# Performance work log

Measured on AMD Instinct MI355X. Metric: run time of the kernel, lower is better.

The kernel has to match this reference:

```python
import jax, jax.numpy as jnp
import numpy as np

N_NODES = 20000
N_EDGES = 320000
F_IN = 256      # num_features_mol
HIDDEN = 512    # hidden_size


def _glorot(key, shape):
    fan_in, fan_out = shape
    lim = jnp.sqrt(6.0 / (fan_in + fan_out)).astype(jnp.float32)
    return jax.random.uniform(key, shape, jnp.float32, -lim, lim)


def setup_inputs() -> dict:
    key = jax.random.key(0)
    ks = jax.random.split(key, 12)
    x = jax.random.normal(ks[0], (N_NODES, F_IN), jnp.float32)
    edge_index = jax.random.randint(ks[1], (2, N_EDGES), 0, N_NODES, dtype=jnp.int64)
    d1, d2, d3 = F_IN * 2, F_IN * 2, F_IN * 4  # 512, 512, 1024
    return {
        "x": x,
        "edge_index": edge_index,
        # SAGEConv layer i: lin_l (neighbor, with bias), lin_r (root, no bias)
        "Wl1": _glorot(ks[2], (F_IN, d1)), "bl1": jnp.zeros((d1,), jnp.float32),
        "Wr1": _glorot(ks[3], (F_IN, d1)),
        "Wl2": _glorot(ks[4], (d1, d2)), "bl2": jnp.zeros((d2,), jnp.float32),
        "Wr2": _glorot(ks[5], (d1, d2)),
        "Wl3": _glorot(ks[6], (d2, d3)), "bl3": jnp.zeros((d3,), jnp.float32),
        "Wr3": _glorot(ks[7], (d2, d3)),
        # mol_fc_g1: Linear(4*F -> hidden)
        "Wfc": _glorot(ks[8], (d3, HIDDEN)), "bfc": jnp.zeros((HIDDEN,), jnp.float32),
    }


def _sage_mean(x, src, dst, Wl, bl, Wr):
    # mean-aggregate neighbor features: messages flow src -> dst
    msg = x[src]                                               # [E, d]
    agg = jax.ops.segment_sum(msg, dst, num_segments=N_NODES)  # [N, d]
    cnt = jax.ops.segment_sum(jnp.ones((src.shape[0],), x.dtype), dst,
                              num_segments=N_NODES)            # [N]
    mean = agg / jnp.maximum(cnt, 1.0)[:, None]                # zero-deg -> 0
    return mean @ Wl + bl + x @ Wr


def reference(x, edge_index, Wl1, bl1, Wr1, Wl2, bl2, Wr2, Wl3, bl3, Wr3, Wfc, bfc):
    src, dst = edge_index[0], edge_index[1]
    h = jax.nn.relu(_sage_mean(x, src, dst, Wl1, bl1, Wr1))
    h = jax.nn.relu(_sage_mean(h, src, dst, Wl2, bl2, Wr2))
    h = jax.nn.relu(_sage_mean(h, src, dst, Wl3, bl3, Wr3))
    return h @ Wfc + bfc                                       # [N, HIDDEN]
```

## Files before the change

kernel.cpp:

```cpp
#include <hip/hip_runtime.h>
#include <hip/hip_bf16.h>


typedef __bf16 bf16x8 __attribute__((ext_vector_type(8)));
typedef float  f32x4  __attribute__((ext_vector_type(4)));

#define N_NODES 20000
#define N_EDGES 320000
#define MPAD 20096

__device__ __forceinline__ int clampi(int v, int lo, int hi) {
    return v < lo ? lo : (v > hi ? hi : v);
}

__device__ __forceinline__ void load16_lds(const void* g, void* l) {
    __builtin_amdgcn_global_load_lds(
        (const __attribute__((address_space(1))) void*)g,
        (__attribute__((address_space(3))) void*)l, 16, 0, 0);
}


__global__ void k_count(const int* __restrict__ ei, int E, int* __restrict__ cnt) {
    int e = blockIdx.x * blockDim.x + threadIdx.x;
    if (e < E) atomicAdd(&cnt[clampi(ei[E + e], 0, N_NODES - 1)], 1);
}

__global__ __launch_bounds__(1024) void k_scan_block(const int* __restrict__ cnt,
                                                     int* __restrict__ off,
                                                     int* __restrict__ bsum, int n) {
    __shared__ int sm[1024];
    int b = blockIdx.x, tid = threadIdx.x;
    int i = b * 1024 + tid;
    int v = (i < n) ? cnt[i] : 0;
    sm[tid] = v;
    __syncthreads();
    for (int s = 1; s < 1024; s <<= 1) {
        int t = (tid >= s) ? sm[tid - s] : 0;
        __syncthreads();
        sm[tid] += t;
        __syncthreads();
    }
    if (i < n) off[i] = sm[tid] - v;
    if (tid == 1023) bsum[b] = sm[1023];
}

__global__ void k_scan_carry(const int* __restrict__ bsum, int* __restrict__ carry,
                             int nb, int* __restrict__ off, int n) {
    if (threadIdx.x == 0 && blockIdx.x == 0) {
        int acc = 0;
        for (int b = 0; b < nb; ++b) { carry[b] = acc; acc += bsum[b]; }
        off[n] = acc;
    }
}

__global__ __launch_bounds__(1024) void k_scan_add(int* __restrict__ off,
                                                   int* __restrict__ cur,
                                                   const int* __restrict__ carry, int n) {
    int i = blockIdx.x * 1024 + threadIdx.x;
    if (i < n) {
        int v = off[i] + carry[blockIdx.x];
        off[i] = v;
        cur[i] = v;
    }
}

__global__ void k_fill(const int* __restrict__ ei, int E,
                       int* __restrict__ cur, int* __restrict__ csr) {
    int e = blockIdx.x * blockDim.x + threadIdx.x;
    if (e < E) {
        int dst = clampi(ei[E + e], 0, N_NODES - 1);
        int src = clampi(ei[e], 0, N_NODES - 1);
        int pos = atomicAdd(&cur[dst], 1);
        if (pos >= 0 && pos < E) csr[pos] = src;
    }
}


struct TDesc { const float* W; __bf16* Wt; int K, N, KT, koff, tile0; };
struct TDescs { TDesc d[7]; };

__global__ void k_transpose_all(TDescs ds) {
    __shared__ float tile[32][33];
    int b = blockIdx.x;
    int di = 0;
#pragma unroll
    for (int i = 1; i < 7; ++i)
        if (b >= ds.d[i].tile0) di = i;
    const float* W = ds.d[di].W;
    __bf16* Wt = ds.d[di].Wt;
    int N = ds.d[di].N, KT = ds.d[di].KT, koff = ds.d[di].koff;
    int t = b - ds.d[di].tile0;
    int ntn = N >> 5;
    int nb = (t % ntn) * 32, kb = (t / ntn) * 32;
    for (int i = 0; i < 32; i += 8) {
        int k = kb + threadIdx.y + i, n = nb + threadIdx.x;
        tile[threadIdx.y + i][threadIdx.x] = W[(size_t)k * N + n];
    }
    __syncthreads();
    for (int i = 0; i < 32; i += 8) {
        int n = nb + threadIdx.y + i, k = koff + kb + threadIdx.x;
        size_t o = (size_t)(n >> 7) * ((size_t)KT * 128) + (size_t)(k >> 3) * 1024 +
                   (size_t)((n & 127) * 8) + (k & 7);
        Wt[o] = (__bf16)tile[threadIdx.x][threadIdx.y + i];
    }
}


__global__ __launch_bounds__(256) void k_agg_f32(const float* __restrict__ xin,
                                                 const int* __restrict__ off,
                                                 const int* __restrict__ csr,
                                                 __bf16* __restrict__ acat) {
    __shared__ float sm[4][256];
    int node = blockIdx.x;
    int tid = threadIdx.x, slot = tid >> 6, lane = tid & 63;
    int c0 = lane * 4;
    int beg = off[node], end = off[node + 1];
    float a0 = 0.f, a1 = 0.f, a2 = 0.f, a3 = 0.f;
    for (int e = beg + slot; e < end; e += 4) {
        int s = csr[e];
        float4 v = *(const float4*)(xin + (size_t)s * 256 + c0);
        a0 += v.x; a1 += v.y; a2 += v.z; a3 += v.w;
    }
    sm[slot][c0] = a0; sm[slot][c0 + 1] = a1; sm[slot][c0 + 2] = a2; sm[slot][c0 + 3] = a3;
    __syncthreads();
    __bf16* base = acat + (size_t)(node >> 7) * (512 * 128) + (size_t)((node & 127) * 8);
    if (tid < 32) {
        float inv = 1.f / fmaxf((float)(end - beg), 1.f);
        int c = tid;
        __bf16 tmp[8];
#pragma unroll
        for (int i = 0; i < 8; ++i) {
            int col = c * 8 + i;
            tmp[i] = (__bf16)((sm[0][col] + sm[1][col] + sm[2][col] + sm[3][col]) * inv);
        }
        *(uint4*)(base + (size_t)c * 1024) = *(const uint4*)tmp;
    } else if (tid >= 64 && tid < 96) {
        int c = tid - 64;
        float4 u = *(const float4*)(xin + (size_t)node * 256 + c * 8);
        float4 w = *(const float4*)(xin + (size_t)node * 256 + c * 8 + 4);
        __bf16 tmp[8] = {(__bf16)u.x, (__bf16)u.y, (__bf16)u.z, (__bf16)u.w,
                         (__bf16)w.x, (__bf16)w.y, (__bf16)w.z, (__bf16)w.w};
        *(uint4*)(base + (size_t)(32 + c) * 1024) = *(const uint4*)tmp;
    }
}

__global__ __launch_bounds__(256) void k_agg_bf16(const __hip_bfloat16* __restrict__ hrm,
                                                  const int* __restrict__ off,
                                                  const int* __restrict__ csr,
                                                  __bf16* __restrict__ acat) {
    __shared__ float sm[4][512];
    int node = blockIdx.x;
    int tid = threadIdx.x, slot = tid >> 6, lane = tid & 63;
    int c0 = lane * 8;
    int beg = off[node], end = off[node + 1];
    float a[8] = {};
    for (int e = beg + slot; e < end; e += 4) {
        int s = csr[e];
        uint4 v = *(const uint4*)(hrm + (size_t)s * 512 + c0);
        const __hip_bfloat16* hb = (const __hip_bfloat16*)&v;
#pragma unroll
        for (int j = 0; j < 8; ++j) a[j] += __bfloat162float(hb[j]);
    }
#pragma unroll
    for (int j = 0; j < 8; ++j) sm[slot][c0 + j] = a[j];
    __syncthreads();
    if (tid < 64) {
        float inv = 1.f / fmaxf((float)(end - beg), 1.f);
        int c = tid;
        __bf16 tmp[8];
#pragma unroll
        for (int i = 0; i < 8; ++i) {
            int col = c * 8 + i;
            tmp[i] = (__bf16)((sm[0][col] + sm[1][col] + sm[2][col] + sm[3][col]) * inv);
        }
        *(uint4*)(acat + (size_t)(node >> 7) * (1024 * 128) +
                  (size_t)((node & 127) * 8) + (size_t)c * 1024) = *(const uint4*)tmp;
    }
}


template <bool RELU, int OUTMODE>
__global__ __launch_bounds__(256) void k_gemm(const __bf16* __restrict__ A, int K, int M,
                                              const __bf16* __restrict__ B,
                                              const float* __restrict__ bias,
                                              __bf16* __restrict__ osw, int Kc, int coff,
                                              __bf16* __restrict__ orm, int ldrm,
                                              float* __restrict__ of32, int ldf,
                                              int rtiles, int ctlog2) {
    constexpr int SMEM = (OUTMODE == 2) ? 34816 : 32768;
    __shared__ char smem[SMEM];
    __bf16* Alds = (__bf16*)smem;
    __bf16* Blds = (__bf16*)(smem + 16384);

    int bid = blockIdx.x;
    int xcd = bid & 7, local = bid >> 3;
    int cmask = (1 << ctlog2) - 1;
    int colTile = local & cmask;
    int rowTile = (local >> ctlog2) * 8 + xcd;
    if (rowTile >= rtiles) return;

    const __bf16* Atile = A + (size_t)rowTile * ((size_t)K * 128);
    const __bf16* Btile = B + (size_t)colTile * ((size_t)K * 128);

    int tid = threadIdx.x;
    int wave = tid >> 6, lane = tid & 63;
    int wr = wave >> 1, wc = wave & 1;
    int quad = lane >> 4, l16 = lane & 15;

    f32x4 acc[4][4] = {};

    for (int k0 = 0; k0 < K; k0 += 64) {
        __syncthreads();
        const __bf16* gA = Atile + (size_t)k0 * 128;
        const __bf16* gB = Btile + (size_t)k0 * 128;
#pragma unroll
        for (int j = 0; j < 4; ++j) {
            int slot = (j * 256 + tid) * 8;
            load16_lds(gA + slot, Alds + slot);
            load16_lds(gB + slot, Blds + slot);
        }
        __syncthreads();
#pragma unroll
        for (int sp = 0; sp < 2; ++sp) {
            bf16x8 af[4], bf[4];
#pragma unroll
            for (int mi = 0; mi < 4; ++mi)
                af[mi] = *(const bf16x8*)(Alds + sp * 4096 + quad * 1024 +
                                          (wr * 64 + mi * 16 + l16) * 8);
#pragma unroll
            for (int ni = 0; ni < 4; ++ni)
                bf[ni] = *(const bf16x8*)(Blds + sp * 4096 + quad * 1024 +
                                          (wc * 64 + ni * 16 + l16) * 8);
#pragma unroll
            for (int mi = 0; mi < 4; ++mi)
#pragma unroll
                for (int ni = 0; ni < 4; ++ni)
                    acc[mi][ni] = __builtin_amdgcn_mfma_f32_16x16x32_bf16(
                        af[mi], bf[ni], acc[mi][ni], 0, 0, 0);
        }
    }

    int col0 = colTile * 128;
    int row0 = rowTile * 128;
    __syncthreads();

    if (OUTMODE != 2) {
        __bf16* cb = (__bf16*)smem;
#pragma unroll
        for (int ni = 0; ni < 4; ++ni) {
            int ct = wc * 64 + ni * 16 + l16;
            float bv = bias[col0 + ct];
#pragma unroll
            for (int mi = 0; mi < 4; ++mi) {
                int rb = wr * 64 + mi * 16 + quad * 4;
#pragma unroll
                for (int r = 0; r < 4; ++r) {
                    float v = acc[mi][ni][r] + bv;
                    if (RELU) v = fmaxf(v, 0.f);
                    cb[(ct >> 3) * 1024 + (rb + r) * 8 + (ct & 7)] = (__bf16)v;
                }
            }
        }
        __syncthreads();
        __bf16* dst = osw + (size_t)rowTile * ((size_t)Kc * 128) +
                      (size_t)((coff + col0) >> 3) * 1024;
#pragma unroll
        for (int p2 = 0; p2 < 8; ++p2) {
            int idx = (p2 * 256 + tid) * 8;
            *(uint4*)(dst + idx) = *(const uint4*)(cb + idx);
        }
        if (OUTMODE == 1) {
#pragma unroll
            for (int p2 = 0; p2 < 8; ++p2) {
                int rr = p2 * 16 + (tid >> 4);
                int cc = tid & 15;
                *(uint4*)(orm + (size_t)(row0 + rr) * ldrm + col0 + cc * 8) =
                    *(const uint4*)(cb + cc * 1024 + rr * 8);
            }
        }
    } else {
        float* cf = (float*)smem;
#pragma unroll
        for (int h = 0; h < 2; ++h) {
            if (wc == h) {
#pragma unroll
                for (int ni = 0; ni < 4; ++ni) {
                    int ctl = ni * 16 + l16;
                    float bv = bias[col0 + h * 64 + ctl];
#pragma unroll
                    for (int mi = 0; mi < 4; ++mi) {
                        int rb = wr * 64 + mi * 16 + quad * 4;
#pragma unroll
                        for (int r = 0; r < 4; ++r) {
                            float v = acc[mi][ni][r] + bv;
                            if (RELU) v = fmaxf(v, 0.f);
                            cf[(rb + r) * 68 + ctl] = v;
                        }
                    }
                }
            }
            __syncthreads();
            int chunk = tid & 15, rl = tid >> 4;
#pragma unroll
            for (int p2 = 0; p2 < 8; ++p2) {
                int rt = p2 * 16 + rl;
                int row = row0 + rt;
                if (row < M) {
                    float4 v = *(const float4*)(cf + rt * 68 + chunk * 4);
                    *(float4*)(of32 + (size_t)row * ldf + col0 + h * 64 + chunk * 4) = v;
                }
            }
            __syncthreads();
        }
    }
}


extern "C" void kernel_launch(void* const* d_in, const int* in_sizes, int n_in,
                              void* d_out, int out_size, void* d_ws, size_t ws_size,
                              hipStream_t stream) {
    const float* x   = (const float*)d_in[0];
    const int*   ei  = (const int*)d_in[1];
    const float* Wl1 = (const float*)d_in[2];
    const float* bl1 = (const float*)d_in[3];
    const float* Wr1 = (const float*)d_in[4];
    const float* Wl2 = (const float*)d_in[5];
    const float* bl2 = (const float*)d_in[6];
    const float* Wr2 = (const float*)d_in[7];
    const float* Wl3 = (const float*)d_in[8];
    const float* bl3 = (const float*)d_in[9];
    const float* Wr3 = (const float*)d_in[10];
    const float* Wfc = (const float*)d_in[11];
    const float* bfc = (const float*)d_in[12];
    float* out = (float*)d_out;

    const int NN = N_NODES, E = N_EDGES;
    const int NB = (NN + 1023) / 1024;

    char* p = (char*)d_ws;
    auto alloc = [&](size_t bytes) {
        char* r = p;
        p += (bytes + 511) & ~(size_t)511;
        return r;
    };
    int* cnt   = (int*)alloc((size_t)NN * 4);
    int* off   = (int*)alloc((size_t)(NN + 1) * 4);
    int* cur   = (int*)alloc((size_t)NN * 4);
    int* csr   = (int*)alloc((size_t)E * 4);
    int* bsum  = (int*)alloc((size_t)NB * 4);
    int* carry = (int*)alloc((size_t)NB * 4);
    __bf16* Acat1 = (__bf16*)alloc((size_t)MPAD * 512 * 2);
    __bf16* Acat2 = (__bf16*)alloc((size_t)MPAD * 1024 * 2);
    __bf16* Acat3 = (__bf16*)alloc((size_t)MPAD * 1024 * 2);
    __bf16* Hrm   = (__bf16*)alloc((size_t)MPAD * 512 * 2);
    __bf16* Wt1 = (__bf16*)alloc((size_t)512 * 512 * 2);
    __bf16* Wt2 = (__bf16*)alloc((size_t)512 * 1024 * 2);
    __bf16* Wt3 = (__bf16*)alloc((size_t)1024 * 1024 * 2);
    __bf16* Wt4 = (__bf16*)alloc((size_t)512 * 1024 * 2);
    __bf16* H3 = Acat2;

    hipMemsetAsync(cnt, 0, (size_t)NN * 4, stream);
    k_count<<<(E + 255) / 256, 256, 0, stream>>>(ei, E, cnt);
    k_scan_block<<<NB, 1024, 0, stream>>>(cnt, off, bsum, NN);
    k_scan_carry<<<1, 64, 0, stream>>>(bsum, carry, NB, off, NN);
    k_scan_add<<<NB, 1024, 0, stream>>>(off, cur, carry, NN);
    k_fill<<<(E + 255) / 256, 256, 0, stream>>>(ei, E, cur, csr);

    TDescs td;
    td.d[0] = {Wl1, Wt1, 256, 512, 512, 0, 0};
    td.d[1] = {Wr1, Wt1, 256, 512, 512, 256, 128};
    td.d[2] = {Wl2, Wt2, 512, 512, 1024, 0, 256};
    td.d[3] = {Wr2, Wt2, 512, 512, 1024, 512, 512};
    td.d[4] = {Wl3, Wt3, 512, 1024, 1024, 0, 768};
    td.d[5] = {Wr3, Wt3, 512, 1024, 1024, 512, 1280};
    td.d[6] = {Wfc, Wt4, 1024, 512, 1024, 0, 1792};
    k_transpose_all<<<2304, dim3(32, 8), 0, stream>>>(td);

    int rtiles = (NN + 127) / 128;
    int rg = ((rtiles + 7) / 8) * 8;

    k_agg_f32<<<NN, 256, 0, stream>>>(x, off, csr, Acat1);
    k_gemm<true, 1><<<rg * 4, 256, 0, stream>>>(
        Acat1, 512, NN, Wt1, bl1, Acat2, 1024, 512, Hrm, 512, nullptr, 0, rtiles, 2);

    k_agg_bf16<<<NN, 256, 0, stream>>>((const __hip_bfloat16*)Hrm, off, csr, Acat2);
    k_gemm<true, 1><<<rg * 4, 256, 0, stream>>>(
        Acat2, 1024, NN, Wt2, bl2, Acat3, 1024, 512, Hrm, 512, nullptr, 0, rtiles, 2);

    k_agg_bf16<<<NN, 256, 0, stream>>>((const __hip_bfloat16*)Hrm, off, csr, Acat3);
    k_gemm<true, 0><<<rg * 8, 256, 0, stream>>>(
        Acat3, 1024, NN, Wt3, bl3, H3, 1024, 0, nullptr, 0, nullptr, 0, rtiles, 3);

    k_gemm<false, 2><<<rg * 4, 256, 0, stream>>>(
        H3, 1024, NN, Wt4, bfc, nullptr, 0, 0, nullptr, 0, out, 512, rtiles, 2);
}
```

Measured before the change: 449.9 us.

## Pre-convert x to bf16 and use one wave per node in aggregation

Adds a kernel that converts the fp32 input features to a row-major bf16 copy and writes the root half of the first concat buffer. Layer-1 aggregation then gathers bf16 rows instead of fp32, halving gather bytes. All aggregation kernels switch from one block per node with a 4-way LDS reduction to one wave per node that walks its edge list sequentially, two edges per iteration. This removes shared-memory reductions and block syncs but lowers per-node memory parallelism for high-degree nodes and adds an extra conversion pass.

```diff
diff --git a/kernel.cpp b/kernel.cpp
--- a/kernel.cpp
+++ b/kernel.cpp
@@ -106,75 +106,69 @@
 }
 
 
-__global__ __launch_bounds__(256) void k_agg_f32(const float* __restrict__ xin,
-                                                 const int* __restrict__ off,
-                                                 const int* __restrict__ csr,
-                                                 __bf16* __restrict__ acat) {
-    __shared__ float sm[4][256];
-    int node = blockIdx.x;
-    int tid = threadIdx.x, slot = tid >> 6, lane = tid & 63;
-    int c0 = lane * 4;
+__global__ __launch_bounds__(256) void k_x2bf(const float* __restrict__ x,
+                                              __bf16* __restrict__ xrm,
+                                              __bf16* __restrict__ acat) {
+    int tid = threadIdx.x;
+    int node = blockIdx.x * 8 + (tid >> 5);
+    int f0 = (tid & 31) * 8;
+    float4 u = *(const float4*)(x + (size_t)node * 256 + f0);
+    float4 w = *(const float4*)(x + (size_t)node * 256 + f0 + 4);
+    alignas(16) __bf16 tmp[8] = {(__bf16)u.x, (__bf16)u.y, (__bf16)u.z, (__bf16)u.w,
+                                 (__bf16)w.x, (__bf16)w.y, (__bf16)w.z, (__bf16)w.w};
+    *(uint4*)(xrm + (size_t)node * 256 + f0) = *(const uint4*)tmp;
+    *(uint4*)(acat + (size_t)(node >> 7) * (512 * 128) +
+              (size_t)(32 + (f0 >> 3)) * 1024 + (size_t)((node & 127) * 8)) =
+        *(const uint4*)tmp;
+}
+
+
+template <int D, int KC>
+__global__ __launch_bounds__(256) void k_agg(const __hip_bfloat16* __restrict__ hrm,
+                                             const int* __restrict__ off,
+                                             const int* __restrict__ csr,
+                                             __bf16* __restrict__ acat) {
+    constexpr int FPL = D / 64;
+    int wave = threadIdx.x >> 6, lane = threadIdx.x & 63;
+    int node = blockIdx.x * 4 + wave;
+    int c0 = lane * FPL;
     int beg = off[node], end = off[node + 1];
-    float a0 = 0.f, a1 = 0.f, a2 = 0.f, a3 = 0.f;
-    for (int e = beg + slot; e < end; e += 4) {
-        int s = csr[e];
-        float4 v = *(const float4*)(xin + (size_t)s * 256 + c0);
-        a0 += v.x; a1 += v.y; a2 += v.z; a3 += v.w;
-    }
-    sm[slot][c0] = a0; sm[slot][c0 + 1] = a1; sm[slot][c0 + 2] = a2; sm[slot][c0 + 3] = a3;
-    __syncthreads();
-    __bf16* base = acat + (size_t)(node >> 7) * (512 * 128) + (size_t)((node & 127) * 8);
-    if (tid < 32) {
-        float inv = 1.f / fmaxf((float)(end - beg), 1.f);
-        int c = tid;
-        __bf16 tmp[8];
-#pragma unroll
-        for (int i = 0; i < 8; ++i) {
-            int col = c * 8 + i;
-            tmp[i] = (__bf16)((sm[0][col] + sm[1][col] + sm[2][col] + sm[3][col]) * inv);
-        }
-        *(uint4*)(base + (size_t)c * 1024) = *(const uint4*)tmp;
-    } else if (tid >= 64 && tid < 96) {
-        int c = tid - 64;
-        float4 u = *(const float4*)(xin + (size_t)node * 256 + c * 8);
-        float4 w = *(const float4*)(xin + (size_t)node * 256 + c * 8 + 4);
-        __bf16 tmp[8] = {(__bf16)u.x, (__bf16)u.y, (__bf16)u.z, (__bf16)u.w,
-                         (__bf16)w.x, (__bf16)w.y, (__bf16)w.z, (__bf16)w.w};
-        *(uint4*)(base + (size_t)(32 + c) * 1024) = *(const uint4*)tmp;
-    }
-}
-
-__global__ __launch_bounds__(256) void k_agg_bf16(const __hip_bfloat16* __restrict__ hrm,
-                                                  const int* __restrict__ off,
-                                                  const int* __restrict__ csr,
-                                                  __bf16* __restrict__ acat) {
-    __shared__ float sm[4][512];
-    int node = blockIdx.x;
-    int tid = threadIdx.x, slot = tid >> 6, lane = tid & 63;
-    int c0 = lane * 8;
-    int beg = off[node], end = off[node + 1];
-    float a[8] = {};
-    for (int e = beg + slot; e < end; e += 4) {
-        int s = csr[e];
-        uint4 v = *(const uint4*)(hrm + (size_t)s * 512 + c0);
-        const __hip_bfloat16* hb = (const __hip_bfloat16*)&v;
+    float a[FPL] = {};
+
+    auto accum = [&](int s) {
+        if constexpr (FPL == 8) {
+            uint4 v = *(const uint4*)(hrm + (size_t)s * D + c0);
+            const __hip_bfloat16* hb = (const __hip_bfloat16*)&v;
 #pragma unroll
         for (int j = 0; j < 8; ++j) a[j] += __bfloat162float(hb[j]);
-    }
-#pragma unroll
-    for (int j = 0; j < 8; ++j) sm[slot][c0 + j] = a[j];
-    __syncthreads();
-    if (tid < 64) {
-        float inv = 1.f / fmaxf((float)(end - beg), 1.f);
-        int c = tid;
-        __bf16 tmp[8];
-#pragma unroll
-        for (int i = 0; i < 8; ++i) {
-            int col = c * 8 + i;
-            tmp[i] = (__bf16)((sm[0][col] + sm[1][col] + sm[2][col] + sm[3][col]) * inv);
-        }
-        *(uint4*)(acat + (size_t)(node >> 7) * (1024 * 128) +
-                  (size_t)((node & 127) * 8) + (size_t)c * 1024) = *(const uint4*)tmp;
+        } else {
+            uint2 v = *(const uint2*)(hrm + (size_t)s * D + c0);
+            const __hip_bfloat16* hb = (const __hip_bfloat16*)&v;
+#pragma unroll
+            for (int j = 0; j < 4; ++j) a[j] += __bfloat162float(hb[j]);
+        }
+    };
+
+    int e = beg;
+    for (; e + 1 < end; e += 2) {
+        int s0 = csr[e], s1 = csr[e + 1];
+        accum(s0);
+        accum(s1);
+    }
+    if (e < end) accum(csr[e]);
+
+    float inv = 1.f / fmaxf((float)(end - beg), 1.f);
+    alignas(16) __bf16 tmp[FPL];
+#pragma unroll
+    for (int j = 0; j < FPL; ++j) tmp[j] = (__bf16)(a[j] * inv);
+
+    __bf16* base = acat + (size_t)(node >> 7) * ((size_t)KC * 128) +
+                   (size_t)((node & 127) * 8);
+    if constexpr (FPL == 8) {
+        *(uint4*)(base + (size_t)lane * 1024) = *(const uint4*)tmp;
+    } else {
+        *(uint2*)(base + (size_t)(lane >> 1) * 1024 + (size_t)((lane & 1) * 4)) =
+            *(const uint2*)tmp;
     }
 }
 
@@ -353,11 +347,14 @@
     __bf16* Acat2 = (__bf16*)alloc((size_t)MPAD * 1024 * 2);
     __bf16* Acat3 = (__bf16*)alloc((size_t)MPAD * 1024 * 2);
     __bf16* Hrm   = (__bf16*)alloc((size_t)MPAD * 512 * 2);
+    __bf16* Xrm   = (__bf16*)alloc((size_t)MPAD * 256 * 2);
     __bf16* Wt1 = (__bf16*)alloc((size_t)512 * 512 * 2);
     __bf16* Wt2 = (__bf16*)alloc((size_t)512 * 1024 * 2);
     __bf16* Wt3 = (__bf16*)alloc((size_t)1024 * 1024 * 2);
     __bf16* Wt4 = (__bf16*)alloc((size_t)512 * 1024 * 2);
     __bf16* H3 = Acat2;
+
+    k_x2bf<<<NN / 8, 256, 0, stream>>>(x, Xrm, Acat1);
 
     hipMemsetAsync(cnt, 0, (size_t)NN * 4, stream);
     k_count<<<(E + 255) / 256, 256, 0, stream>>>(ei, E, cnt);
@@ -379,15 +376,18 @@
     int rtiles = (NN + 127) / 128;
     int rg = ((rtiles + 7) / 8) * 8;
 
-    k_agg_f32<<<NN, 256, 0, stream>>>(x, off, csr, Acat1);
+    k_agg<256, 512><<<NN / 4, 256, 0, stream>>>(
+        (const __hip_bfloat16*)Xrm, off, csr, Acat1);
     k_gemm<true, 1><<<rg * 4, 256, 0, stream>>>(
         Acat1, 512, NN, Wt1, bl1, Acat2, 1024, 512, Hrm, 512, nullptr, 0, rtiles, 2);
 
-    k_agg_bf16<<<NN, 256, 0, stream>>>((const __hip_bfloat16*)Hrm, off, csr, Acat2);
+    k_agg<512, 1024><<<NN / 4, 256, 0, stream>>>(
+        (const __hip_bfloat16*)Hrm, off, csr, Acat2);
     k_gemm<true, 1><<<rg * 4, 256, 0, stream>>>(
         Acat2, 1024, NN, Wt2, bl2, Acat3, 1024, 512, Hrm, 512, nullptr, 0, rtiles, 2);
 
-    k_agg_bf16<<<NN, 256, 0, stream>>>((const __hip_bfloat16*)Hrm, off, csr, Acat3);
+    k_agg<512, 1024><<<NN / 4, 256, 0, stream>>>(
+        (const __hip_bfloat16*)Hrm, off, csr, Acat3);
     k_gemm<true, 0><<<rg * 8, 256, 0, stream>>>(
         Acat3, 1024, NN, Wt3, bl3, H3, 1024, 0, nullptr, 0, nullptr, 0, rtiles, 3);
 
```

Result: faster. 417.4 us (-7.2%).
